# Kernel optimization log

Hardware: AMD Instinct MI355X
Metric: run time of the kernel (lower is better)

## Reference

```python
import jax, jax.numpy as jnp
import numpy as np

DIM = 512
NUM_HEADS = 8
HEAD_DIM = DIM // NUM_HEADS
FFN_DIM = 4 * DIM
EPS = 1e-6


def rmsnorm(x, w):
    rms = jnp.sqrt(jnp.mean(x * x, axis=-1, keepdims=True) + EPS)
    return x / rms * w


def setup_inputs() -> dict:
    key = jax.random.key(0)
    ks = jax.random.split(key, 8)
    B, T = 4, 2048
    x = jax.random.normal(ks[0], (B, T, DIM), dtype=jnp.float32)
    # Linear weights stored as [in, out] (transpose of torch layout)
    w_qkv = jax.random.normal(ks[1], (DIM, 3 * DIM), dtype=jnp.float32) * 0.02
    w_out = jax.random.normal(ks[2], (DIM, DIM), dtype=jnp.float32) * 0.02
    b_out = jnp.zeros((DIM,), dtype=jnp.float32)
    w1 = jax.random.normal(ks[3], (DIM, FFN_DIM), dtype=jnp.float32) * 0.02
    b1 = jnp.zeros((FFN_DIM,), dtype=jnp.float32)
    w2 = jax.random.normal(ks[4], (FFN_DIM, DIM), dtype=jnp.float32) * 0.02
    b2 = jnp.zeros((DIM,), dtype=jnp.float32)
    norm1_w = jnp.ones((DIM,), dtype=jnp.float32)
    norm2_w = jnp.ones((DIM,), dtype=jnp.float32)
    return {
        "x": x, "norm1_w": norm1_w, "norm2_w": norm2_w,
        "w_qkv": w_qkv, "w_out": w_out, "b_out": b_out,
        "w1": w1, "b1": b1, "w2": w2, "b2": b2,
        "context_size": 64,
    }


def reference(x, norm1_w, norm2_w, w_qkv, w_out, b_out, w1, b1, w2, b2, context_size):
    B, T, D = x.shape
    H, Hd = NUM_HEADS, HEAD_DIM
    # --- attention sublayer ---
    xn = rmsnorm(x, norm1_w)
    qkv = xn @ w_qkv                      # (B, T, 3D)
    q, k, v = jnp.split(qkv, 3, axis=-1)
    q = q.reshape(B, T, H, Hd).transpose(0, 2, 1, 3)  # (B, H, T, Hd)
    k = k.reshape(B, T, H, Hd).transpose(0, 2, 1, 3)
    v = v.reshape(B, T, H, Hd).transpose(0, 2, 1, 3)
    scale = Hd ** -0.5
    scores = jnp.einsum('bhqd,bhkd->bhqk', q, k) * scale  # (B, H, T, T)
    idx = jnp.arange(T)
    band = jnp.abs(idx[:, None] - idx[None, :]) <= context_size  # (T, T)
    scores = jnp.where(band[None, None], scores, -jnp.inf)
    attn = jax.nn.softmax(scores, axis=-1)
    out = jnp.einsum('bhqk,bhkd->bhqd', attn, v)  # (B, H, T, Hd)
    out = out.transpose(0, 2, 1, 3).reshape(B, T, D)
    out = out @ w_out + b_out
    x = x + out
    # --- FFN sublayer ---
    h = rmsnorm(x, norm2_w)
    h = jax.nn.gelu(h @ w1 + b1, approximate=False)
    x = x + (h @ w2 + b2)
    return x
```

## Files before the change

kernel.cpp:

```cpp
#include <hip/hip_runtime.h>
#include <cstdint>
#include <cstddef>

#define B_  4
#define T_  2048
#define D_  512
#define NH_ 8
#define HD_ 64
#define FF_ 2048
#define M_  (B_*T_)

typedef unsigned short u16;
typedef __attribute__((ext_vector_type(8))) unsigned short u16x8;
typedef __attribute__((ext_vector_type(8))) __bf16         bf16x8;
typedef __attribute__((ext_vector_type(4))) float          f32x4;

__device__ __forceinline__ u16 f2bf(float f) {
  unsigned u = __float_as_uint(f);
  u += 0x7FFF + ((u >> 16) & 1);
  return (u16)(u >> 16);
}
__device__ __forceinline__ float bf2f(u16 h) {
  return __uint_as_float((unsigned)h << 16);
}

__device__ __forceinline__ f32x4 mfma_bf16(u16x8 a, u16x8 b, f32x4 c) {
  return __builtin_amdgcn_mfma_f32_16x16x32_bf16(
      __builtin_bit_cast(bf16x8, a), __builtin_bit_cast(bf16x8, b), c, 0, 0, 0);
}

__device__ __forceinline__ void async16(const void* g, void* l) {
  __builtin_amdgcn_global_load_lds(
      (const __attribute__((address_space(1))) unsigned int*)g,
      (__attribute__((address_space(3))) unsigned int*)l, 16, 0, 0);
}

__device__ __forceinline__ float gelu_f(float v) {
  float ax = fabsf(v) * 0.70710678118f;
  float t = 1.0f / (1.0f + 0.3275911f * ax);
  float p = ((((1.061405429f * t - 1.453152027f) * t + 1.421413741f) * t
              - 0.284496736f) * t + 0.254829592f) * t;
  float e = __expf(-ax * ax);
  float er = 1.0f - p * e;
  float s = (v >= 0.0f) ? er : -er;
  return 0.5f * v * (1.0f + s);
}

__global__ __launch_bounds__(256) void prep_kernel(
    const float* __restrict__ i0, u16* __restrict__ o0,
    const float* __restrict__ i1, u16* __restrict__ o1,
    const float* __restrict__ i2, u16* __restrict__ o2,
    const float* __restrict__ i3, u16* __restrict__ o3,
    const float* __restrict__ x, const float* __restrict__ n1w,
    const float* __restrict__ n2w,
    float* __restrict__ inv, u16* __restrict__ xbf, float* __restrict__ ssz) {
  __shared__ float tile[32][33];
  const int bid = blockIdx.x, tid = threadIdx.x;
  if (bid < 3072) {
    const float* in; u16* out; const float* sc; int R, C, gx, lb;
    if (bid < 768)       { in = i0; out = o0; R = 512;  C = 1536; gx = 48; lb = bid;        sc = n1w; }
    else if (bid < 1024) { in = i1; out = o1; R = 512;  C = 512;  gx = 16; lb = bid - 768;  sc = nullptr; }
    else if (bid < 2048) { in = i2; out = o2; R = 512;  C = 2048; gx = 64; lb = bid - 1024; sc = n2w; }
    else                 { in = i3; out = o3; R = 2048; C = 512;  gx = 16; lb = bid - 2048; sc = nullptr; }
    int c0 = (lb % gx) * 32, r0 = (lb / gx) * 32;
    int tx = tid & 31, ty = tid >> 5;
#pragma unroll
    for (int i = 0; i < 4; i++)
      tile[ty + i * 8][tx] = in[(size_t)(r0 + ty + i * 8) * C + c0 + tx];
    __syncthreads();
    float s = sc ? sc[r0 + tx] : 1.0f;
#pragma unroll
    for (int i = 0; i < 4; i++)
      out[(size_t)(c0 + ty + i * 8) * R + r0 + tx] = f2bf(tile[tx][ty + i * 8] * s);
  } else if (bid < 5120) {
    int row  = (bid - 3072) * 4 + (tid >> 6);
    int lane = tid & 63;
    const float* xr = x + (size_t)row * D_ + lane * 8;
    float v[8];
    *(float4*)(v)     = *(const float4*)xr;
    *(float4*)(v + 4) = *(const float4*)(xr + 4);
    u16 rw[8];
#pragma unroll
    for (int e = 0; e < 8; e++) rw[e] = f2bf(v[e]);
    *(uint4*)(xbf + (size_t)row * D_ + lane * 8) = *(uint4*)rw;
    float ss = 0.f;
#pragma unroll
    for (int e = 0; e < 8; e++) ss += v[e] * v[e];
#pragma unroll
    for (int m = 1; m < 64; m <<= 1) ss += __shfl_xor(ss, m, 64);
    if (lane == 0) inv[row] = rsqrtf(ss * (1.0f / D_) + 1e-6f);
  } else {
    ssz[(bid - 5120) * 256 + tid] = 0.f;
  }
}

template <bool HAS_BIAS, int SCALE_MODE, bool DO_GELU>
__global__ __launch_bounds__(512) void gemm256_kernel(
    const u16* __restrict__ A, const u16* __restrict__ Bt, u16* __restrict__ C,
    const float* __restrict__ bias, const float* __restrict__ rowscale,
    int M, int N, int K) {
  extern __shared__ __align__(16) char dsmem[];
  const int tid = threadIdx.x;
  const int lane = tid & 63, w = tid >> 6;
  const int quad = lane >> 4, m16 = lane & 15;
  const int wm = w & 1, wn = w >> 1;
  const int nbx = N >> 8;
  const int wg  = blockIdx.x;
  const int xcd = wg & 7, slot = wg >> 3;
  const int mper = (M >> 8) >> 3;
  const int mloc = slot / nbx, nxp = slot - mloc * nbx;
  const int m0 = (xcd * mper + mloc) << 8, n0 = nxp << 8;

  const int srow = tid >> 3;
  const int scol = ((tid & 7) ^ (srow & 7)) * 8;
  const u16* Ag = A  + (size_t)(m0 + srow) * K + scol;
  const u16* Bg = Bt + (size_t)(n0 + srow) * K + scol;

  auto stA = [&](int bsel, int kt, int half) {
    char* d = dsmem + bsel * 32768 + half * 16384 + tid * 16;
#pragma unroll
    for (int c = 0; c < 2; c++)
      async16(Ag + (size_t)(half * 128 + c * 64) * K + kt * 64, d + c * 8192);
  };
  auto stB = [&](int bsel, int kt, int half) {
    char* d = dsmem + 65536 + bsel * 32768 + half * 16384 + tid * 16;
#pragma unroll
    for (int c = 0; c < 2; c++)
      async16(Bg + (size_t)(half * 128 + c * 64) * K + kt * 64, d + c * 8192);
  };

  f32x4 acc[8][4];
#pragma unroll
  for (int i = 0; i < 8; i++)
#pragma unroll
    for (int j = 0; j < 4; j++) acc[i][j] = (f32x4){0.f, 0.f, 0.f, 0.f};

  const int nk = K >> 6, nt = nk >> 1;
  stA(0, 0, 0); stA(0, 0, 1); stB(0, 0, 0); stB(0, 0, 1);
  stA(1, 1, 0); stA(1, 1, 1); stB(1, 1, 0); stB(1, 1, 1);
  asm volatile("s_waitcnt vmcnt(8)" ::: "memory");
  __builtin_amdgcn_s_barrier();

  const u16* lA0 = (const u16*)(dsmem);
  const u16* lA1 = (const u16*)(dsmem + 32768);
  const u16* lB0 = (const u16*)(dsmem + 65536);
  const u16* lB1 = (const u16*)(dsmem + 98304);

  for (int t = 0; t < nt; ++t) {
    const int t2 = t << 1;
    const bool last = (t == nt - 1);
    u16x8 bfr[4][2];
#pragma unroll
    for (int q = 0; q < 4; ++q) {
      if (q == 0) {
#pragma unroll
        for (int j = 0; j < 4; ++j)
#pragma unroll
          for (int kk = 0; kk < 2; ++kk)
            bfr[j][kk] = *(const u16x8*)(lB0 + (wn * 64 + j * 16 + m16) * 64 +
                                         (((kk * 4 + quad) ^ (m16 & 7)) * 8));
      }
      u16x8 af[2][2];
#pragma unroll
      for (int s = 0; s < 2; ++s)
#pragma unroll
        for (int kk = 0; kk < 2; ++kk)
          af[s][kk] = *(const u16x8*)(lA0 + (wm * 128 + (q * 2 + s) * 16 + m16) * 64 +
                                      (((kk * 4 + quad) ^ (m16 & 7)) * 8));
      if (q == 0 && t >= 1) stA(1, t2 + 1, 0);
      if (q == 1) {
        if (t >= 1) stA(1, t2 + 1, 1);
        if (t2 + 2 < nk) stB(0, t2 + 2, 0);
      }
      if (q == 2 && t2 + 2 < nk) stB(0, t2 + 2, 1);
      __builtin_amdgcn_s_barrier();
      asm volatile("s_waitcnt lgkmcnt(0)" ::: "memory");
      __builtin_amdgcn_s_setprio(1);
#pragma unroll
      for (int s = 0; s < 2; ++s)
#pragma unroll
        for (int kk = 0; kk < 2; ++kk)
#pragma unroll
          for (int j = 0; j < 4; ++j)
            acc[q * 2 + s][j] = mfma_bf16(af[s][kk], bfr[j][kk], acc[q * 2 + s][j]);
      __builtin_amdgcn_s_setprio(0);
      if (q == 3) {
        if (last) asm volatile("s_waitcnt vmcnt(0)" ::: "memory");
        else      asm volatile("s_waitcnt vmcnt(4)" ::: "memory");
      }
      __builtin_amdgcn_s_barrier();
    }
#pragma unroll
    for (int q = 0; q < 4; ++q) {
      if (q == 0) {
#pragma unroll
        for (int j = 0; j < 4; ++j)
#pragma unroll
          for (int kk = 0; kk < 2; ++kk)
            bfr[j][kk] = *(const u16x8*)(lB1 + (wn * 64 + j * 16 + m16) * 64 +
                                         (((kk * 4 + quad) ^ (m16 & 7)) * 8));
      }
      u16x8 af[2][2];
#pragma unroll
      for (int s = 0; s < 2; ++s)
#pragma unroll
        for (int kk = 0; kk < 2; ++kk)
          af[s][kk] = *(const u16x8*)(lA1 + (wm * 128 + (q * 2 + s) * 16 + m16) * 64 +
                                      (((kk * 4 + quad) ^ (m16 & 7)) * 8));
      if (q == 0 && t2 + 2 < nk) stA(0, t2 + 2, 0);
      if (q == 1) {
        if (t2 + 2 < nk) stA(0, t2 + 2, 1);
        if (t2 + 3 < nk) stB(1, t2 + 3, 0);
      }
      if (q == 2 && t2 + 3 < nk) stB(1, t2 + 3, 1);
      __builtin_amdgcn_s_barrier();
      asm volatile("s_waitcnt lgkmcnt(0)" ::: "memory");
      __builtin_amdgcn_s_setprio(1);
#pragma unroll
      for (int s = 0; s < 2; ++s)
#pragma unroll
        for (int kk = 0; kk < 2; ++kk)
#pragma unroll
          for (int j = 0; j < 4; ++j)
            acc[q * 2 + s][j] = mfma_bf16(af[s][kk], bfr[j][kk], acc[q * 2 + s][j]);
      __builtin_amdgcn_s_setprio(0);
      if (q == 3 && !last)
        asm volatile("s_waitcnt vmcnt(4)" ::: "memory");
      __builtin_amdgcn_s_barrier();
    }
  }

  __syncthreads();
  float* eps = (float*)dsmem;
  const int ecol = (tid & 31) * 8;
  float bv[8];
  if (HAS_BIAS) {
    *(float4*)(bv)     = *(const float4*)(bias + n0 + ecol);
    *(float4*)(bv + 4) = *(const float4*)(bias + n0 + ecol + 4);
  }
#pragma unroll
  for (int i = 0; i < 8; ++i) {
    __syncthreads();
#pragma unroll
    for (int j = 0; j < 4; ++j)
#pragma unroll
      for (int r = 0; r < 4; ++r)
        eps[(wm * 16 + quad * 4 + r) * 260 + wn * 64 + j * 16 + m16] = acc[i][j][r];
    __syncthreads();
#pragma unroll
    for (int rep = 0; rep < 2; ++rep) {
      const int lr = rep * 16 + (tid >> 5);
      const int rg = m0 + (lr >> 4) * 128 + i * 16 + (lr & 15);
      float v[8];
      *(float4*)(v)     = *(const float4*)(eps + lr * 260 + ecol);
      *(float4*)(v + 4) = *(const float4*)(eps + lr * 260 + ecol + 4);
      if (SCALE_MODE != 0) {
        float rs;
        if (SCALE_MODE == 1) rs = rowscale[rg];
        else                 rs = rsqrtf(rowscale[rg] * (1.0f / D_) + 1e-6f);
#pragma unroll
        for (int e = 0; e < 8; e++) v[e] *= rs;
      }
      if (HAS_BIAS) {
#pragma unroll
        for (int e = 0; e < 8; e++) v[e] += bv[e];
      }
      if (DO_GELU) {
#pragma unroll
        for (int e = 0; e < 8; e++) v[e] = gelu_f(v[e]);
      }
      u16 o[8];
#pragma unroll
      for (int e = 0; e < 8; e++) o[e] = f2bf(v[e]);
      *(uint4*)(C + (size_t)rg * N + n0 + ecol) = *(uint4*)o;
    }
  }
}

template <int BM, int BN, bool HAS_BIAS, int RES_MODE, bool DO_GELU,
          bool STORE_BF16, int SCALE_MODE, bool EMIT_SS>
__global__ __launch_bounds__(256) void gemm_kernel(
    const u16* __restrict__ A, const u16* __restrict__ Bt, void* __restrict__ Cv,
    const float* __restrict__ bias, const void* __restrict__ resv,
    const float* __restrict__ rowscale, float* __restrict__ ssout,
    int M, int N, int K) {
  constexpr int ACH = BM / 32;
  constexpr int BCH = BN / 32;
  constexpr int WM  = BM / 2, WN = BN / 2;
  constexpr int MI  = WM / 16, NJ = WN / 16;
  constexpr int EW  = BN + 4;
  constexpr int STG = (BM + BN) * 128;
  constexpr int EPB = 32 * EW * 4;
  constexpr int SMB = (2 * STG > EPB) ? 2 * STG : EPB;
  __shared__ __align__(16) char smem[SMB];
  const int tid = threadIdx.x;
  const int lane = tid & 63, w = tid >> 6;
  const int quad = lane >> 4, m16 = lane & 15;
  const int wm = w & 1, wn = w >> 1;

  const int nbx  = N / BN;
  const int wg   = blockIdx.x;
  const int xcd  = wg & 7, slot = wg >> 3;
  const int mper = (M / BM) >> 3;
  const int mloc = slot / nbx;
  const int nxp  = slot - mloc * nbx;
  const int m0 = (xcd * mper + mloc) * BM, n0 = nxp * BN;

  f32x4 acc[MI][NJ];
#pragma unroll
  for (int i = 0; i < MI; i++)
#pragma unroll
    for (int j = 0; j < NJ; j++) acc[i][j] = (f32x4){0.f, 0.f, 0.f, 0.f};

  const int srow = tid >> 3;
  const int scol = (((tid & 7) ^ (srow & 7))) * 8;
  const u16* Ag = A  + (size_t)(m0 + srow) * K + scol;
  const u16* Bg = Bt + (size_t)(n0 + srow) * K + scol;

  auto stage = [&](int buf, int kt) {
    char* base = smem + buf * STG;
#pragma unroll
    for (int c = 0; c < ACH; c++)
      async16(Ag + (size_t)c * 32 * K + kt, base + c * 4096 + tid * 16);
#pragma unroll
    for (int c = 0; c < BCH; c++)
      async16(Bg + (size_t)c * 32 * K + kt, base + BM * 128 + c * 4096 + tid * 16);
  };
  auto compute = [&](int buf) {
    const u16* lA = (const u16*)(smem + buf * STG);
    const u16* lB = (const u16*)(smem + buf * STG + BM * 128);
#pragma unroll
    for (int kk = 0; kk < 2; kk++) {
      const int sl = ((kk * 4 + quad) ^ (m16 & 7)) * 8;
      const u16* pa = lA + (wm * WM + m16) * 64 + sl;
      const u16* pb = lB + (wn * WN + m16) * 64 + sl;
      u16x8 af[MI], bfr[NJ];
#pragma unroll
      for (int i = 0; i < MI; i++) af[i] = *(const u16x8*)(pa + i * 1024);
#pragma unroll
      for (int j = 0; j < NJ; j++) bfr[j] = *(const u16x8*)(pb + j * 1024);
#pragma unroll
      for (int i = 0; i < MI; i++)
#pragma unroll
        for (int j = 0; j < NJ; j++)
          acc[i][j] = mfma_bf16(af[i], bfr[j], acc[i][j]);
    }
  };

  const int nk = K >> 6;
  stage(0, 0);
  for (int t = 0; t < nk; t++) {
    __syncthreads();
    if (t + 1 < nk) stage((t + 1) & 1, (t + 1) << 6);
    compute(t & 1);
  }

  float* eps = (float*)smem;
  constexpr int REPS = (32 * BN) / (256 * 8);
  float bv[REPS > 0 ? REPS : 1][8];
  if (HAS_BIAS) {
#pragma unroll
    for (int rep = 0; rep < REPS; rep++) {
      const int col = (BN == 128) ? ((tid & 15) * 8) : ((tid & 7) * 8);
      *(float4*)(bv[rep])     = *(const float4*)(bias + n0 + col);
      *(float4*)(bv[rep] + 4) = *(const float4*)(bias + n0 + col + 4);
    }
  }
#pragma unroll
  for (int i = 0; i < MI; i++) {
    __syncthreads();
#pragma unroll
    for (int j = 0; j < NJ; j++)
#pragma unroll
      for (int r = 0; r < 4; r++)
        eps[(wm * 16 + quad * 4 + r) * EW + wn * WN + j * 16 + m16] =
            acc[i][j][r];
    __syncthreads();
#pragma unroll
    for (int rep = 0; rep < REPS; rep++) {
      const int lr  = (BN == 128) ? (rep * 16 + (tid >> 4)) : (tid >> 3);
      const int col = (BN == 128) ? ((tid & 15) * 8) : ((tid & 7) * 8);
      const int rg  = m0 + (lr >> 4) * WM + i * 16 + (lr & 15);
      float v[8];
      *(float4*)(v)     = *(const float4*)(eps + lr * EW + col);
      *(float4*)(v + 4) = *(const float4*)(eps + lr * EW + col + 4);
      if (SCALE_MODE != 0) {
        float rs;
        if (SCALE_MODE == 1) rs = rowscale[rg];
        else                 rs = rsqrtf(rowscale[rg] * (1.0f / D_) + 1e-6f);
#pragma unroll
        for (int e = 0; e < 8; e++) v[e] *= rs;
      }
      if (HAS_BIAS) {
#pragma unroll
        for (int e = 0; e < 8; e++) v[e] += bv[rep][e];
      }
      if (DO_GELU) {
#pragma unroll
        for (int e = 0; e < 8; e++) v[e] = gelu_f(v[e]);
      }
      const size_t idx = (size_t)rg * N + n0 + col;
      if (RES_MODE == 1) {
        float4 r0 = *(const float4*)((const float*)resv + idx);
        float4 r1 = *(const float4*)((const float*)resv + idx + 4);
        v[0] += r0.x; v[1] += r0.y; v[2] += r0.z; v[3] += r0.w;
        v[4] += r1.x; v[5] += r1.y; v[6] += r1.z; v[7] += r1.w;
      } else if (RES_MODE == 2) {
        u16x8 rr = *(const u16x8*)((const u16*)resv + idx);
#pragma unroll
        for (int e = 0; e < 8; e++) v[e] += bf2f(rr[e]);
      }
      if (EMIT_SS) {
        float ps = 0.f;
#pragma unroll
        for (int e = 0; e < 8; e++) ps += v[e] * v[e];
        ps += __shfl_xor(ps, 1, 64);
        ps += __shfl_xor(ps, 2, 64);
        ps += __shfl_xor(ps, 4, 64);
        ps += __shfl_xor(ps, 8, 64);
        if ((tid & 15) == 0) atomicAdd(ssout + rg, ps);
      }
      if (STORE_BF16) {
        u16 o[8];
#pragma unroll
        for (int e = 0; e < 8; e++) o[e] = f2bf(v[e]);
        *(uint4*)((u16*)Cv + idx) = *(uint4*)o;
      } else {
        *(float4*)((float*)Cv + idx)     = *(float4*)(v);
        *(float4*)((float*)Cv + idx + 4) = *(float4*)(v + 4);
      }
    }
  }
}

#define VP_ 216
__global__ __launch_bounds__(256) void attn_kernel(const u16* __restrict__ qkv,
                                                   u16* __restrict__ out) {
  __shared__ __align__(16) char smem[26624 + 64 * VP_ * 2];
  u16* Ks = (u16*)smem;
  u16* Vt = (u16*)(smem + 26624);
  const int tid = threadIdx.x, lane = tid & 63, w = tid >> 6;
  const int quad = lane >> 4, m16 = lane & 15;
  const int qc = ((blockIdx.x & 7) << 2) | (blockIdx.x >> 3);
  const int q0 = qc * 64, h = blockIdx.y, b = blockIdx.z;
  const int kstart = q0 - 64;
  const u16* base = qkv + (size_t)b * T_ * 1536;

  for (int c = tid; c < 1664; c += 256) {
    int row = c >> 3, ch = c & 7;
    int j = kstart + row;
    j = j < 0 ? 0 : (j > T_ - 1 ? T_ - 1 : j);
    *(uint4*)(Ks + row * 64 + ((ch ^ (row & 7)) * 8)) =
        *(const uint4*)(base + (size_t)j * 1536 + 512 + h * 64 + ch * 8);
  }
  for (int c = tid; c < 1664; c += 256) {
    int row = c >> 3, cc = (c & 7) * 8;
    int j = kstart + row;
    j = j < 0 ? 0 : (j > T_ - 1 ? T_ - 1 : j);
    uint4 u = *(const uint4*)(base + (size_t)j * 1536 + 1024 + h * 64 + cc);
    u16 tmp[8];
    *(uint4*)tmp = u;
#pragma unroll
    for (int i = 0; i < 8; i++) Vt[(cc + i) * VP_ + row] = tmp[i];
  }
  const int qw = q0 + w * 16;
  const u16* qb = base + (size_t)(qw + m16) * 1536 + h * 64 + quad * 8;
  u16x8 a0 = *(const u16x8*)qb;
  u16x8 a1 = *(const u16x8*)(qb + 32);
  __syncthreads();

  float s[10][4];
#pragma unroll
  for (int t = 0; t < 10; t++) {
    int kt = (w + t) * 16;
    int kr = kt + m16, sw = kr & 7;
    u16x8 kb0 = *(const u16x8*)(Ks + kr * 64 + ((quad ^ sw) * 8));
    u16x8 kb1 = *(const u16x8*)(Ks + kr * 64 + (((4 + quad) ^ sw) * 8));
    f32x4 acc = {0.f, 0.f, 0.f, 0.f};
    acc = mfma_bf16(a0, kb0, acc);
    acc = mfma_bf16(a1, kb1, acc);
    int jab = kstart + kt + m16;
#pragma unroll
    for (int r = 0; r < 4; r++) {
      int q = qw + quad * 4 + r;
      int d = q - jab;
      bool valid = (jab >= 0) && (jab < T_) && (d <= 64) && (d >= -64);
      s[t][r] = valid ? acc[r] * 0.125f : -1e30f;
    }
  }
  float mx[4], sm[4];
#pragma unroll
  for (int r = 0; r < 4; r++) mx[r] = -1e30f;
#pragma unroll
  for (int t = 0; t < 10; t++)
#pragma unroll
    for (int r = 0; r < 4; r++) mx[r] = fmaxf(mx[r], s[t][r]);
#pragma unroll
  for (int r = 0; r < 4; r++) {
#pragma unroll
    for (int msk = 1; msk < 16; msk <<= 1)
      mx[r] = fmaxf(mx[r], __shfl_xor(mx[r], msk, 64));
    sm[r] = 0.f;
  }
#pragma unroll
  for (int t = 0; t < 10; t++)
#pragma unroll
    for (int r = 0; r < 4; r++) {
      float e = __expf(s[t][r] - mx[r]);
      s[t][r] = e; sm[r] += e;
    }
#pragma unroll
  for (int r = 0; r < 4; r++) {
#pragma unroll
    for (int msk = 1; msk < 16; msk <<= 1) sm[r] += __shfl_xor(sm[r], msk, 64);
    sm[r] = 1.0f / sm[r];
  }
  __syncthreads();
  u16* Ps = (u16*)smem + w * 2688;
#pragma unroll
  for (int t = 0; t < 10; t++)
#pragma unroll
    for (int r = 0; r < 4; r++)
      Ps[(quad * 4 + r) * 168 + t * 16 + m16] = f2bf(s[t][r] * sm[r]);
  __syncthreads();

  f32x4 o[4];
#pragma unroll
  for (int dt = 0; dt < 4; dt++) o[dt] = (f32x4){0.f, 0.f, 0.f, 0.f};
#pragma unroll
  for (int c5 = 0; c5 < 5; c5++) {
    u16x8 pa = *(const u16x8*)(Ps + m16 * 168 + c5 * 32 + quad * 8);
#pragma unroll
    for (int dt = 0; dt < 4; dt++) {
      u16x8 vb = *(const u16x8*)(Vt + (dt * 16 + m16) * VP_ + w * 16 + c5 * 32 + quad * 8);
      o[dt] = mfma_bf16(pa, vb, o[dt]);
    }
  }
#pragma unroll
  for (int dt = 0; dt < 4; dt++)
#pragma unroll
    for (int r = 0; r < 4; r++)
      out[(size_t)(b * T_ + qw + quad * 4 + r) * D_ + h * HD_ + dt * 16 + m16] =
          f2bf(o[dt][r]);
}

extern "C" void kernel_launch(void* const* d_in, const int* in_sizes, int n_in,
                              void* d_out, int out_size, void* d_ws, size_t ws_size,
                              hipStream_t stream) {
  (void)in_sizes; (void)n_in; (void)out_size; (void)ws_size;
  const float* x     = (const float*)d_in[0];
  const float* n1w   = (const float*)d_in[1];
  const float* n2w   = (const float*)d_in[2];
  const float* w_qkv = (const float*)d_in[3];
  const float* w_out = (const float*)d_in[4];
  const float* b_out = (const float*)d_in[5];
  const float* w1    = (const float*)d_in[6];
  const float* b1    = (const float*)d_in[7];
  const float* w2    = (const float*)d_in[8];
  const float* b2    = (const float*)d_in[9];
  float* out = (float*)d_out;
  char* ws = (char*)d_ws;

  u16* wqkvT  = (u16*)(ws + 0);
  u16* woutT  = (u16*)(ws + 1572864);
  u16* w1T    = (u16*)(ws + 2097152);
  u16* w2T    = (u16*)(ws + 4194304);
  float* inv  = (float*)(ws + 6291456);
  float* sums = (float*)(ws + 6324224);
  u16* qkv    = (u16*)(ws + 14680064);
  u16* attno  = (u16*)(ws + 39845888);
  u16* x1     = (u16*)(ws + 48234496);
  u16* xbf    = (u16*)(ws + 56623104);
  u16* hbuf   = qkv;

  static bool cfg = false;
  if (!cfg) {
    hipFuncSetAttribute((const void*)gemm256_kernel<false, 1, false>,
                        hipFuncAttributeMaxDynamicSharedMemorySize, 131072);
    hipFuncSetAttribute((const void*)gemm256_kernel<true, 2, true>,
                        hipFuncAttributeMaxDynamicSharedMemorySize, 131072);
    cfg = true;
  }

  prep_kernel<<<5152, 256, 0, stream>>>(
      w_qkv, wqkvT, w_out, woutT, w1, w1T, w2, w2T, x, n1w, n2w, inv, xbf, sums);

  gemm256_kernel<false, 1, false><<<192, 512, 131072, stream>>>(
      xbf, wqkvT, qkv, nullptr, inv, M_, 3 * D_, D_);
  attn_kernel<<<dim3(32, 8, 4), 256, 0, stream>>>(qkv, attno);
  gemm_kernel<64, 128, true, 2, false, true, 0, true>
      <<<dim3(4 * 128), 256, 0, stream>>>(
      attno, woutT, (void*)x1, b_out, xbf, nullptr, sums, M_, D_, D_);
  gemm256_kernel<true, 2, true><<<256, 512, 131072, stream>>>(
      x1, w1T, hbuf, b1, sums, M_, FF_, D_);
  gemm_kernel<64, 128, true, 2, false, false, 0, false>
      <<<dim3(4 * 128), 256, 0, stream>>>(
      hbuf, w2T, (void*)out, b2, x1, nullptr, nullptr, M_, D_, FF_);
}
```

Baseline: 202.6 us.

## Replace atomic sum-of-squares with per-tile partials, relax GEMM barriers, async K loads

The out-projection GEMM now writes its per-row sum-of-squares partial for each column tile into a separate slot instead of using atomicAdd. This removes the zeroing pass in the prep kernel and the atomic contention, and the FFN1 GEMM sums the four partials when it computes the RMS scale. The small GEMM's main loop swaps __syncthreads for an explicit vmcnt wait plus raw barriers, so the next stage's loads stay in flight across the barrier. The attention kernel loads K with async global-to-LDS copies. The vmcnt literal is hard-coded to six loads per stage, which makes correctness depend on the tile configuration and on the compiler's ordering.

```diff
diff --git a/kernel.cpp b/kernel.cpp
--- a/kernel.cpp
+++ b/kernel.cpp
@@ -53,7 +53,7 @@
     const float* __restrict__ i3, u16* __restrict__ o3,
     const float* __restrict__ x, const float* __restrict__ n1w,
     const float* __restrict__ n2w,
-    float* __restrict__ inv, u16* __restrict__ xbf, float* __restrict__ ssz) {
+    float* __restrict__ inv, u16* __restrict__ xbf) {
   __shared__ float tile[32][33];
   const int bid = blockIdx.x, tid = threadIdx.x;
   if (bid < 3072) {
@@ -72,7 +72,7 @@
 #pragma unroll
     for (int i = 0; i < 4; i++)
       out[(size_t)(c0 + ty + i * 8) * R + r0 + tx] = f2bf(tile[tx][ty + i * 8] * s);
-  } else if (bid < 5120) {
+  } else {
     int row  = (bid - 3072) * 4 + (tid >> 6);
     int lane = tid & 63;
     const float* xr = x + (size_t)row * D_ + lane * 8;
@@ -89,8 +89,6 @@
 #pragma unroll
     for (int m = 1; m < 64; m <<= 1) ss += __shfl_xor(ss, m, 64);
     if (lane == 0) inv[row] = rsqrtf(ss * (1.0f / D_) + 1e-6f);
-  } else {
-    ssz[(bid - 5120) * 256 + tid] = 0.f;
   }
 }
 
@@ -256,8 +254,13 @@
       *(float4*)(v + 4) = *(const float4*)(eps + lr * 260 + ecol + 4);
       if (SCALE_MODE != 0) {
         float rs;
-        if (SCALE_MODE == 1) rs = rowscale[rg];
-        else                 rs = rsqrtf(rowscale[rg] * (1.0f / D_) + 1e-6f);
+        if (SCALE_MODE == 1)      rs = rowscale[rg];
+        else if (SCALE_MODE == 2) rs = rsqrtf(rowscale[rg] * (1.0f / D_) + 1e-6f);
+        else {
+          float s4 = rowscale[rg] + rowscale[M_ + rg] +
+                     rowscale[2 * M_ + rg] + rowscale[3 * M_ + rg];
+          rs = rsqrtf(s4 * (1.0f / D_) + 1e-6f);
+        }
 #pragma unroll
         for (int e = 0; e < 8; e++) v[e] *= rs;
       }
@@ -292,6 +295,7 @@
   constexpr int STG = (BM + BN) * 128;
   constexpr int EPB = 32 * EW * 4;
   constexpr int SMB = (2 * STG > EPB) ? 2 * STG : EPB;
+  static_assert(ACH + BCH == 6, "vmcnt literal assumes 6 loads per stage");
   __shared__ __align__(16) char smem[SMB];
   const int tid = threadIdx.x;
   const int lane = tid & 63, w = tid >> 6;
@@ -350,9 +354,15 @@
   const int nk = K >> 6;
   stage(0, 0);
   for (int t = 0; t < nk; t++) {
-    __syncthreads();
-    if (t + 1 < nk) stage((t + 1) & 1, (t + 1) << 6);
+    if (t + 1 < nk) {
+      stage((t + 1) & 1, (t + 1) << 6);
+      asm volatile("s_waitcnt vmcnt(6)" ::: "memory");
+    } else {
+      asm volatile("s_waitcnt vmcnt(0)" ::: "memory");
+    }
+    __builtin_amdgcn_s_barrier();
     compute(t & 1);
+    __builtin_amdgcn_s_barrier();
   }
 
   float* eps = (float*)smem;
@@ -418,7 +428,7 @@
         ps += __shfl_xor(ps, 2, 64);
         ps += __shfl_xor(ps, 4, 64);
         ps += __shfl_xor(ps, 8, 64);
-        if ((tid & 15) == 0) atomicAdd(ssout + rg, ps);
+        if ((tid & 15) == 0) ssout[(size_t)nxp * M + rg] = ps;
       }
       if (STORE_BF16) {
         u16 o[8];
@@ -446,12 +456,22 @@
   const int kstart = q0 - 64;
   const u16* base = qkv + (size_t)b * T_ * 1536;
 
-  for (int c = tid; c < 1664; c += 256) {
-    int row = c >> 3, ch = c & 7;
+#pragma unroll
+  for (int r6 = 0; r6 < 6; r6++) {
+    int c = r6 * 256 + tid;
+    int row = c >> 3;
     int j = kstart + row;
     j = j < 0 ? 0 : (j > T_ - 1 ? T_ - 1 : j);
-    *(uint4*)(Ks + row * 64 + ((ch ^ (row & 7)) * 8)) =
-        *(const uint4*)(base + (size_t)j * 1536 + 512 + h * 64 + ch * 8);
+    int srcch = ((c & 7) ^ (row & 7)) * 8;
+    async16(base + (size_t)j * 1536 + 512 + h * 64 + srcch, smem + c * 16);
+  }
+  if (tid < 128) {
+    int c = 1536 + tid;
+    int row = c >> 3;
+    int j = kstart + row;
+    j = j < 0 ? 0 : (j > T_ - 1 ? T_ - 1 : j);
+    int srcch = ((c & 7) ^ (row & 7)) * 8;
+    async16(base + (size_t)j * 1536 + 512 + h * 64 + srcch, smem + c * 16);
   }
   for (int c = tid; c < 1664; c += 256) {
     int row = c >> 3, cc = (c & 7) * 8;
@@ -566,7 +586,7 @@
   u16* w1T    = (u16*)(ws + 2097152);
   u16* w2T    = (u16*)(ws + 4194304);
   float* inv  = (float*)(ws + 6291456);
-  float* sums = (float*)(ws + 6324224);
+  float* sums4= (float*)(ws + 6324224);
   u16* qkv    = (u16*)(ws + 14680064);
   u16* attno  = (u16*)(ws + 39845888);
   u16* x1     = (u16*)(ws + 48234496);
@@ -577,22 +597,22 @@
   if (!cfg) {
     hipFuncSetAttribute((const void*)gemm256_kernel<false, 1, false>,
                         hipFuncAttributeMaxDynamicSharedMemorySize, 131072);
-    hipFuncSetAttribute((const void*)gemm256_kernel<true, 2, true>,
+    hipFuncSetAttribute((const void*)gemm256_kernel<true, 3, true>,
                         hipFuncAttributeMaxDynamicSharedMemorySize, 131072);
     cfg = true;
   }
 
-  prep_kernel<<<5152, 256, 0, stream>>>(
-      w_qkv, wqkvT, w_out, woutT, w1, w1T, w2, w2T, x, n1w, n2w, inv, xbf, sums);
+  prep_kernel<<<5120, 256, 0, stream>>>(
+      w_qkv, wqkvT, w_out, woutT, w1, w1T, w2, w2T, x, n1w, n2w, inv, xbf);
 
   gemm256_kernel<false, 1, false><<<192, 512, 131072, stream>>>(
       xbf, wqkvT, qkv, nullptr, inv, M_, 3 * D_, D_);
   attn_kernel<<<dim3(32, 8, 4), 256, 0, stream>>>(qkv, attno);
   gemm_kernel<64, 128, true, 2, false, true, 0, true>
       <<<dim3(4 * 128), 256, 0, stream>>>(
-      attno, woutT, (void*)x1, b_out, xbf, nullptr, sums, M_, D_, D_);
-  gemm256_kernel<true, 2, true><<<256, 512, 131072, stream>>>(
-      x1, w1T, hbuf, b1, sums, M_, FF_, D_);
+      attno, woutT, (void*)x1, b_out, xbf, nullptr, sums4, M_, D_, D_);
+  gemm256_kernel<true, 3, true><<<256, 512, 131072, stream>>>(
+      x1, w1T, hbuf, b1, sums4, M_, FF_, D_);
   gemm_kernel<64, 128, true, 2, false, false, 0, false>
       <<<dim3(4 * 128), 256, 0, stream>>>(
       hbuf, w2T, (void*)out, b2, x1, nullptr, nullptr, M_, D_, FF_);
```

Measured after the change: 196.5 us. 1.03x faster.
